# Kernel optimization log

Measured on AMD Instinct MI355X. Metric: run time of the kernel, lower is better.

Reference implementation:

```python
import jax, jax.numpy as jnp
import numpy as np

N_CRYST = 256   # number of crystals
A = 64          # atoms per crystal (uniform)
K = 20          # max_neighbors
HID = 128       # hidden_dim (emb_size_atom/edge)
LAT = 256       # latent_dim
NRBF = 128      # radial basis size
NBLK = 3        # interaction blocks
CUTOFF = 6.0    # radius
N_ATOMS = N_CRYST * A
E = N_ATOMS * K


def _lattice(lengths, angles):
    # lengths, angles: (N_cryst, 3); angles in degrees -> (N_cryst, 3, 3) row-vector lattice
    rad = angles * (np.pi / 180.0)
    cos = jnp.cos(rad)
    sg = jnp.sin(rad[:, 2])
    a, b, c = lengths[:, 0], lengths[:, 1], lengths[:, 2]
    cx = c * cos[:, 1]
    cy = c * (cos[:, 0] - cos[:, 1] * cos[:, 2]) / sg
    cz = jnp.sqrt(jnp.maximum(c ** 2 - cx ** 2 - cy ** 2, 1e-8))
    zeros = jnp.zeros_like(a)
    v1 = jnp.stack([a, zeros, zeros], -1)
    v2 = jnp.stack([b * cos[:, 2], b * sg, zeros], -1)
    v3 = jnp.stack([cx, cy, cz], -1)
    return jnp.stack([v1, v2, v3], axis=1)


def setup_inputs() -> dict:
    key = jax.random.key(0)
    ks = jax.random.split(key, 20)
    z = jax.random.normal(ks[0], (N_CRYST, LAT), jnp.float32)
    frac_coords = jax.random.uniform(ks[1], (N_ATOMS, 3), jnp.float32)
    lengths = 5.0 + 10.0 * jax.random.uniform(ks[2], (N_CRYST, 3), jnp.float32)
    angles = 60.0 + 60.0 * jax.random.uniform(ks[3], (N_CRYST, 3), jnp.float32)
    atom_types = jax.random.randint(ks[4], (N_ATOMS,), 1, 101)
    src = jnp.repeat(jnp.arange(N_ATOMS), K)
    dst = (src // A) * A + jax.random.randint(ks[5], (E,), 0, A)

    def w(k, shape, fan):
        return jax.random.normal(k, shape, jnp.float32) / np.sqrt(fan)

    params = dict(
        emb_table=w(ks[6], (101, HID), 1.0),
        W_in=w(ks[7], (HID + LAT, HID), HID + LAT), b_in=jnp.zeros((HID,), jnp.float32),
        W_edge=w(ks[8], (2 * HID + NRBF, HID), 2 * HID + NRBF), b_edge=jnp.zeros((HID,), jnp.float32),
        Wb_rbf=w(ks[9], (NBLK, NRBF, HID), NRBF),
        Wb_msg=w(ks[10], (NBLK, HID, HID), HID), bb_msg=jnp.zeros((NBLK, HID), jnp.float32),
        Wb_atom=w(ks[11], (NBLK, HID, HID), HID), bb_atom=jnp.zeros((NBLK, HID), jnp.float32),
        Wb_upd=w(ks[12], (NBLK, 3 * HID, HID), 3 * HID), bb_upd=jnp.zeros((NBLK, HID), jnp.float32),
        W_force=w(ks[13], (HID, 1), HID), b_force=jnp.zeros((1,), jnp.float32),
        W_fc1=w(ks[14], (HID, HID), HID), b_fc1=jnp.zeros((HID,), jnp.float32),
        W_fc2=w(ks[15], (HID, HID), HID), b_fc2=jnp.zeros((HID,), jnp.float32),
        W_fc3=w(ks[16], (HID, 2), HID), b_fc3=jnp.zeros((2,), jnp.float32),
    )
    return dict(z=z, frac_coords=frac_coords, lengths=lengths, angles=angles,
                atom_types=atom_types, src=src, dst=dst, **params)


def reference(z, frac_coords, lengths, angles,
              emb_table, W_in, b_in, W_edge, b_edge,
              Wb_rbf, Wb_msg, bb_msg, Wb_atom, bb_atom, Wb_upd, bb_upd,
              W_force, b_force, W_fc1, b_fc1, W_fc2, b_fc2, W_fc3, b_fc3,
              atom_types, src, dst):
    batch_idx = jnp.arange(N_ATOMS) // A  # crystal id per atom
    lattice = _lattice(lengths, angles)   # (N_cryst,3,3)
    cart = jnp.einsum('ni,nij->nj', frac_coords, lattice[batch_idx])  # (N_atoms,3)

    dvec = cart[dst] - cart[src]                        # (E,3)
    dist = jnp.sqrt(jnp.sum(dvec * dvec, -1) + 1e-12)    # (E,)
    unit = dvec / dist[:, None]

    mu = jnp.linspace(0.0, CUTOFF, NRBF)
    delta = CUTOFF / (NRBF - 1)
    env = 0.5 * (jnp.cos(np.pi * jnp.minimum(dist / CUTOFF, 1.0)) + 1.0)  # smooth cutoff
    rbf = jnp.exp(-(((dist[:, None] - mu) / delta) ** 2)) * env[:, None]   # (E,NRBF)

    # atom embedding conditioned on per-crystal latent
    h = jax.nn.relu(jnp.concatenate([emb_table[atom_types], z[batch_idx]], -1) @ W_in + b_in)
    # edge embedding
    m = jax.nn.relu(jnp.concatenate([h[src], h[dst], rbf], -1) @ W_edge + b_edge)

    for i in range(NBLK):
        gate = rbf @ Wb_rbf[i]                                   # (E,HID)
        msg = jax.nn.relu(m @ Wb_msg[i] + bb_msg[i]) * gate       # (E,HID)
        agg = jax.ops.segment_sum(msg, dst, num_segments=N_ATOMS) # (N_atoms,HID)
        h = h + jax.nn.relu(agg @ Wb_atom[i] + bb_atom[i])
        m = m + jax.nn.relu(jnp.concatenate([h[src], h[dst], m], -1) @ Wb_upd[i] + bb_upd[i])

    # per-edge force magnitude projected along edge direction, summed per atom
    f = m @ W_force + b_force                                     # (E,1)
    pred_cart_coord_diff = jax.ops.segment_sum(f * unit, dst, num_segments=N_ATOMS)  # (N_atoms,3)

    a1 = jax.nn.relu(h @ W_fc1 + b_fc1)
    a2 = jax.nn.relu(a1 @ W_fc2 + b_fc2)
    pred_atom_types = a2 @ W_fc3 + b_fc3                          # (N_atoms,2)
    return pred_cart_coord_diff, pred_atom_types
```

## Files before the change

### kernel.cpp

```cpp
#include <hip/hip_runtime.h>
#include <hip/hip_bf16.h>

#define NCRYST 256
#define AATOMS 64
#define KNBR   20
#define HID    128
#define LAT    256
#define NRBF   128
#define NBLK   3
#define NATOMS (NCRYST * AATOMS)
#define NEDGE  (NATOMS * KNBR)
#define NPART  2
#define DQ     4096
#define PI_F   3.14159265358979323846f
#define CUT_F  6.0f
#define CHB    1040

typedef short short8 __attribute__((ext_vector_type(8)));
typedef float f32x4  __attribute__((ext_vector_type(4)));

__device__ __forceinline__ float bf2f(__hip_bfloat16 x) { return __bfloat162float(x); }
__device__ __forceinline__ __hip_bfloat16 f2bf(float x) { return __float2bfloat16(x); }
__device__ __forceinline__ float s2f(short x) {
  return __uint_as_float(((unsigned)(unsigned short)x) << 16);
}
__device__ __forceinline__ short f2s(float x) {
  union { short s; __hip_bfloat16 b; } u; u.b = f2bf(x); return u.s;
}

#define DMA16(gptr, lptr) __builtin_amdgcn_global_load_lds( \
    (const __attribute__((address_space(1))) void*)(gptr),  \
    (__attribute__((address_space(3))) void*)(lptr), 16, 0, 0)

#define WCNT_VM11_LGKM0 0x007B
#define WCNT_VM10_LGKM0 0x007A
#define WCNT_VM4_LGKM0  0x0074
#define WCNT_VM0_LGKM0  0x0070
#define WCNT_LGKM0_ONLY 0xC07F

__global__ void k_cart(const float* __restrict__ frac, const float* __restrict__ lengths,
                       const float* __restrict__ angles, float* __restrict__ cart) {
  int atom = blockIdx.x * blockDim.x + threadIdx.x;
  if (atom >= NATOMS) return;
  int c = atom >> 6;
  float al = angles[c*3+0] * (PI_F/180.f);
  float be = angles[c*3+1] * (PI_F/180.f);
  float ga = angles[c*3+2] * (PI_F/180.f);
  float ca = cosf(al), cb = cosf(be), cg = cosf(ga), sg = sinf(ga);
  float a = lengths[c*3+0], b = lengths[c*3+1], cl = lengths[c*3+2];
  float cx = cl * cb;
  float cy = cl * (ca - cb*cg) / sg;
  float cz = sqrtf(fmaxf(cl*cl - cx*cx - cy*cy, 1e-8f));
  float f0 = frac[atom*3+0], f1 = frac[atom*3+1], f2 = frac[atom*3+2];
  cart[atom*3+0] = f0*a + f1*(b*cg) + f2*cx;
  cart[atom*3+1] = f1*(b*sg) + f2*cy;
  cart[atom*3+2] = f2*cz;
}

__global__ void k_edge(const float* __restrict__ cart, const int* __restrict__ src,
                       const int* __restrict__ dst, float* __restrict__ unit,
                       float* __restrict__ dist, const float* __restrict__ b_force,
                       float* __restrict__ fbuf) {
  int e = blockIdx.x * blockDim.x + threadIdx.x;
  if (e >= NEDGE) return;
  int s = src[e], d = dst[e];
  float dx = cart[d*3+0] - cart[s*3+0];
  float dy = cart[d*3+1] - cart[s*3+1];
  float dz = cart[d*3+2] - cart[s*3+2];
  float dd = sqrtf(dx*dx + dy*dy + dz*dz + 1e-12f);
  float inv = 1.f / dd;
  dist[e] = dd;
  unit[e*3+0] = dx*inv; unit[e*3+1] = dy*inv; unit[e*3+2] = dz*inv;
  fbuf[e] = b_force[0];
}

__global__ __launch_bounds__(128) void k_tab(const float* __restrict__ W_edge,
                                             const float* __restrict__ Wb_rbf,
                                             float* __restrict__ T) {
  int q = blockIdx.x, n = threadIdx.x;
  __shared__ float rv[128];
  float d = (float)q * (CUT_F / (float)(DQ - 1));
  float env = 0.5f * (cosf(PI_F * fminf(d * (1.f/CUT_F), 1.f)) + 1.f);
  float t = (d - (float)n * (CUT_F/(NRBF-1))) * ((NRBF-1)/CUT_F);
  rv[n] = expf(-t*t) * env;
  __syncthreads();
  float a0 = 0.f, a1 = 0.f, a2 = 0.f, a3 = 0.f;
  for (int j = 0; j < 128; ++j) {
    float r = rv[j];
    a0 = fmaf(r, W_edge[(256 + j)*128 + n], a0);
    a1 = fmaf(r, Wb_rbf[0*16384 + j*128 + n], a1);
    a2 = fmaf(r, Wb_rbf[1*16384 + j*128 + n], a2);
    a3 = fmaf(r, Wb_rbf[2*16384 + j*128 + n], a3);
  }
  T[(0*DQ + q)*128 + n] = a0;
  T[(1*DQ + q)*128 + n] = a1;
  T[(2*DQ + q)*128 + n] = a2;
  T[(3*DQ + q)*128 + n] = a3;
}

__global__ void k_wcast(const float* __restrict__ W_in, const float* __restrict__ W_edge,
                        const float* __restrict__ Wb_upd, const float* __restrict__ Wb_msg,
                        const float* __restrict__ Wb_atom, const float* __restrict__ W_fc1,
                        const float* __restrict__ W_fc2, __hip_bfloat16* __restrict__ WT) {
  int idx = blockIdx.x * 256 + threadIdx.x;
  if (idx >= 360448) return;
  if (idx < 49152) {
    int n = idx / 384, k = idx % 384;
    WT[idx] = f2bf(W_in[k*128 + n]);
    return;
  }
  int t = idx - 49152;
  int b = t >> 14, q = t & 16383;
  int n = q >> 7, k = q & 127;
  const float* S; int krow;
  if (b == 0)       { S = W_edge; krow = k; }
  else if (b == 1)  { S = W_edge; krow = 128 + k; }
  else if (b <= 10) { int i = (b-2)/3, part = (b-2)%3;
                      S = Wb_upd + i*49152; krow = part*128 + k; }
  else if (b <= 13) { S = Wb_msg + (b-11)*16384; krow = k; }
  else if (b <= 16) { S = Wb_atom + (b-14)*16384; krow = k; }
  else if (b == 17) { S = W_fc1; krow = k; }
  else              { S = W_fc2; krow = k; }
  WT[idx] = f2bf(S[krow*128 + n]);
}

__global__ __launch_bounds__(256) void k_hm(
    const int* __restrict__ atype, const float* __restrict__ z,
    const float* __restrict__ emb, const __hip_bfloat16* __restrict__ WTin,
    const float* __restrict__ b, float* __restrict__ h,
    __hip_bfloat16* __restrict__ h_bf) {
  const int tid = threadIdx.x;
  const int w = tid >> 6, lane = tid & 63, ln = lane & 15, qd = lane >> 4;
  const int row0w = blockIdx.x * 64 + w * 16;
  const int arow = row0w + ln;
  const float* esrc = emb + (size_t)atype[arow] * 128;
  const float* zsrc = z + (size_t)(arow >> 6) * LAT;

  short8 af[12];
#pragma unroll
  for (int ks = 0; ks < 4; ++ks) {
    float4 v0 = *(const float4*)(esrc + ks*32 + qd*8);
    float4 v1 = *(const float4*)(esrc + ks*32 + qd*8 + 4);
    af[ks] = (short8){f2s(v0.x),f2s(v0.y),f2s(v0.z),f2s(v0.w),
                      f2s(v1.x),f2s(v1.y),f2s(v1.z),f2s(v1.w)};
  }
#pragma unroll
  for (int ks = 4; ks < 12; ++ks) {
    float4 v0 = *(const float4*)(zsrc + (ks-4)*32 + qd*8);
    float4 v1 = *(const float4*)(zsrc + (ks-4)*32 + qd*8 + 4);
    af[ks] = (short8){f2s(v0.x),f2s(v0.y),f2s(v0.z),f2s(v0.w),
                      f2s(v1.x),f2s(v1.y),f2s(v1.z),f2s(v1.w)};
  }

  const short* Wb = (const short*)WTin + ln*384 + qd*8;
  f32x4 acc[8];
#pragma unroll
  for (int ct = 0; ct < 8; ++ct) acc[ct] = (f32x4){0,0,0,0};
#pragma unroll
  for (int ks = 0; ks < 12; ++ks)
#pragma unroll
    for (int ct = 0; ct < 8; ++ct)
      acc[ct] = __builtin_amdgcn_mfma_f32_16x16x32_bf16(af[ks],
                  *(const short8*)(Wb + ct*16*384 + ks*32), acc[ct], 0,0,0);

#pragma unroll
  for (int ct = 0; ct < 8; ++ct) {
    int col = ct*16 + ln;
    float bias = b[col];
#pragma unroll
    for (int reg = 0; reg < 4; ++reg) {
      int crow = row0w + qd*4 + reg;
      float v = fmaxf(acc[ct][reg] + bias, 0.f);
      size_t o = (size_t)crow*128 + col;
      h[o] = v;
      h_bf[o] = f2bf(v);
    }
  }
}

__global__ __launch_bounds__(256) void k_uv2(
    const __hip_bfloat16* __restrict__ A,
    const __hip_bfloat16* __restrict__ WT1, const __hip_bfloat16* __restrict__ WT2,
    __hip_bfloat16* __restrict__ O1, __hip_bfloat16* __restrict__ O2) {
  const int tid = threadIdx.x;
  const int w = tid >> 6, lane = tid & 63, ln = lane & 15, qd = lane >> 4;
  const int row0w = blockIdx.x * 64 + w * 16;
  const int arow = row0w + ln;

  short8 af[4];
  const short* pa = (const short*)A + (size_t)arow*128 + qd*8;
#pragma unroll
  for (int ks = 0; ks < 4; ++ks) af[ks] = *(const short8*)(pa + ks*32);

  f32x4 a1[8], a2[8];
#pragma unroll
  for (int ct = 0; ct < 8; ++ct) { a1[ct] = (f32x4){0,0,0,0}; a2[ct] = (f32x4){0,0,0,0}; }
#pragma unroll
  for (int ct = 0; ct < 8; ++ct) {
    const short* b1 = (const short*)WT1 + (ct*16 + ln)*128 + qd*8;
    const short* b2 = (const short*)WT2 + (ct*16 + ln)*128 + qd*8;
#pragma unroll
    for (int ks = 0; ks < 4; ++ks) {
      a1[ct] = __builtin_amdgcn_mfma_f32_16x16x32_bf16(af[ks], *(const short8*)(b1 + ks*32), a1[ct], 0,0,0);
      a2[ct] = __builtin_amdgcn_mfma_f32_16x16x32_bf16(af[ks], *(const short8*)(b2 + ks*32), a2[ct], 0,0,0);
    }
  }
#pragma unroll
  for (int ct = 0; ct < 8; ++ct) {
    int col = ct*16 + ln;
#pragma unroll
    for (int reg = 0; reg < 4; ++reg) {
      size_t o = (size_t)(row0w + qd*4 + reg)*128 + col;
      O1[o] = f2bf(a1[ct][reg]);
      O2[o] = f2bf(a2[ct][reg]);
    }
  }
}

__global__ __launch_bounds__(256) void k_minit(
    const int* __restrict__ src, const int* __restrict__ dst,
    const float* __restrict__ dist,
    const __hip_bfloat16* __restrict__ u0, const __hip_bfloat16* __restrict__ v0,
    const float* __restrict__ T0, const float* __restrict__ b,
    __hip_bfloat16* __restrict__ m) {
  const int t = threadIdx.x;
  const int li = t & 15, ei = t >> 4;
  float bcol[8];
#pragma unroll
  for (int u = 0; u < 8; ++u) bcol[u] = b[li*8 + u];

  int e[4]; float dd[4]; short8 us[4], vs[4];
#pragma unroll
  for (int g = 0; g < 4; ++g) {
    e[g] = blockIdx.x*64 + g*16 + ei;
    dd[g] = dist[e[g]];
    int s = src[e[g]], d = dst[e[g]];
    us[g] = *(const short8*)((const short*)u0 + (size_t)s*128 + li*8);
    vs[g] = *(const short8*)((const short*)v0 + (size_t)d*128 + li*8);
  }
  float t0v[4][8], t1v[4][8]; float fr[4]; bool in[4];
#pragma unroll
  for (int g = 0; g < 4; ++g) {
    in[g] = dd[g] < CUT_F;
    float x = fminf(dd[g], CUT_F) * ((float)(DQ - 1) / CUT_F);
    int i0 = (int)x;
    fr[g] = x - (float)i0;
    const float* tp = T0 + (size_t)i0*128 + li*8;
    *(float4*)&t0v[g][0] = *(const float4*)tp;
    *(float4*)&t0v[g][4] = *(const float4*)(tp + 4);
    *(float4*)&t1v[g][0] = *(const float4*)(tp + 128);
    *(float4*)&t1v[g][4] = *(const float4*)(tp + 132);
  }
#pragma unroll
  for (int g = 0; g < 4; ++g) {
    short8 o;
#pragma unroll
    for (int u = 0; u < 8; ++u) {
      float tv = in[g] ? fmaf(fr[g], t1v[g][u] - t0v[g][u], t0v[g][u]) : 0.f;
      float v = s2f(us[g][u]) + s2f(vs[g][u]) + tv + bcol[u];
      o[u] = f2s(fmaxf(v, 0.f));
    }
    *(uint4*)((short*)m + (size_t)e[g]*128 + li*8) = *(uint4*)&o;
  }
}

template<int MODE>
__global__ __launch_bounds__(256) void k_eup(
    const int* __restrict__ src, const int* __restrict__ dst,
    __hip_bfloat16* __restrict__ m,
    const __hip_bfloat16* __restrict__ uu, const __hip_bfloat16* __restrict__ vv,
    const __hip_bfloat16* __restrict__ WTmm, const float* __restrict__ b,
    const float* __restrict__ Wf, float* __restrict__ fout) {
  __shared__ short Bs[128 * 132];
  __shared__ __align__(16) char Abuf[2][17 * CHB];
  __shared__ short srcS[640], dstS[640];
  const int tid = threadIdx.x;
  const int w = tid >> 6, lane = tid & 63, ln = lane & 15, qd = lane >> 4;
  const int cg = w & 1, rh = w >> 1;
  const int e_loc = lane >> 4;
  const int sgc = (lane & 15) ^ (e_loc << 2);
  const int cry = blockIdx.x >> 1, half = blockIdx.x & 1;
  const int ebase = cry * 1280 + half * 640;
  const int ca = cry * 64;

#pragma unroll
  for (int i = 0; i < 8; ++i) {
    int g = i * 256 + tid;
    int colb = g >> 4, ch = g & 15;
    *(uint4*)&Bs[colb*132 + ch*8] = ((const uint4*)((const short*)WTmm + colb*128))[ch];
  }
  for (int i = tid; i < 640; i += 256) {
    srcS[i] = (short)(src[ebase + i] & 63);
    dstS[i] = (short)(dst[ebase + i] & 63);
  }

  float bias4[4], wf4[4];
#pragma unroll
  for (int ct = 0; ct < 4; ++ct) bias4[ct] = b[cg*64 + ct*16 + ln];
  if constexpr (MODE == 2) {
#pragma unroll
    for (int ct = 0; ct < 4; ++ct) wf4[ct] = Wf[cg*64 + ct*16 + ln];
  }

  short8 Bu[2][4], Bv[2][4];
#pragma unroll
  for (int ks = 0; ks < 2; ++ks)
#pragma unroll
    for (int ct = 0; ct < 4; ++ct) {
      const int col = cg*64 + ct*16 + ln;
#pragma unroll
      for (int j = 0; j < 8; ++j) {
        const size_t ro = (size_t)(ca + ks*32 + qd*8 + j) * 128 + col;
        Bu[ks][ct][j] = ((const short*)uu)[ro];
        Bv[ks][ct][j] = ((const short*)vv)[ro];
      }
    }

#pragma unroll
  for (int t4 = 0; t4 < 4; ++t4) {
    int chunk = w * 4 + t4;
    const short* gp = (const short*)m + (size_t)(ebase + chunk*4 + e_loc)*128 + sgc*8;
    DMA16(gp, Abuf[0] + chunk * CHB);
  }

  for (int t = 0; t < 10; ++t) {
    const int nb = t & 1;
    if (t < 9) {
#pragma unroll
      for (int t4 = 0; t4 < 4; ++t4) {
        int chunk = w * 4 + t4;
        const short* gp = (const short*)m +
            (size_t)(ebase + (t+1)*64 + chunk*4 + e_loc)*128 + sgc*8;
        DMA16(gp, Abuf[nb^1] + chunk * CHB);
      }
      __builtin_amdgcn_s_waitcnt(WCNT_VM4_LGKM0);
    } else {
      __builtin_amdgcn_s_waitcnt(WCNT_VM0_LGKM0);
    }
    __builtin_amdgcn_s_barrier();

    const char* Ab = Abuf[nb];
    const int e0 = ebase + t*64;
    const int l0 = t*64;

    const int rowA = rh*32 + ln, rowB = rowA + 16;
    const int sa = srcS[l0 + rowA], da = dstS[l0 + rowA];
    const int sb = srcS[l0 + rowB], db = dstS[l0 + rowB];

    f32x4 acc0[4], acc1[4];
#pragma unroll
    for (int ct = 0; ct < 4; ++ct) { acc0[ct] = (f32x4){0,0,0,0}; acc1[ct] = (f32x4){0,0,0,0}; }
    const int sx = (ln & 3) << 2;
#pragma unroll
    for (int ks = 0; ks < 4; ++ks) {
      int slot = ((ks*4 + qd) ^ sx) << 4;
      short8 aA = *(const short8*)(Ab + (rowA>>2)*CHB + (ln&3)*256 + slot);
      short8 aB = *(const short8*)(Ab + (rowB>>2)*CHB + (ln&3)*256 + slot);
#pragma unroll
      for (int ct = 0; ct < 4; ++ct) {
        short8 bb = *(const short8*)&Bs[(cg*64 + ct*16 + ln)*132 + ks*32 + qd*8];
        acc0[ct] = __builtin_amdgcn_mfma_f32_16x16x32_bf16(aA, bb, acc0[ct], 0,0,0);
        acc1[ct] = __builtin_amdgcn_mfma_f32_16x16x32_bf16(aB, bb, acc1[ct], 0,0,0);
      }
    }

#pragma unroll
    for (int ks = 0; ks < 2; ++ks) {
      short8 ohAu, ohAv, ohBu, ohBv;
#pragma unroll
      for (int j = 0; j < 8; ++j) {
        const int kk = ks*32 + qd*8 + j;
        ohAu[j] = (sa == kk) ? (short)0x3F80 : (short)0;
        ohAv[j] = (da == kk) ? (short)0x3F80 : (short)0;
        ohBu[j] = (sb == kk) ? (short)0x3F80 : (short)0;
        ohBv[j] = (db == kk) ? (short)0x3F80 : (short)0;
      }
#pragma unroll
      for (int ct = 0; ct < 4; ++ct) {
        acc0[ct] = __builtin_amdgcn_mfma_f32_16x16x32_bf16(ohAu, Bu[ks][ct], acc0[ct], 0,0,0);
        acc0[ct] = __builtin_amdgcn_mfma_f32_16x16x32_bf16(ohAv, Bv[ks][ct], acc0[ct], 0,0,0);
        acc1[ct] = __builtin_amdgcn_mfma_f32_16x16x32_bf16(ohBu, Bu[ks][ct], acc1[ct], 0,0,0);
        acc1[ct] = __builtin_amdgcn_mfma_f32_16x16x32_bf16(ohBv, Bv[ks][ct], acc1[ct], 0,0,0);
      }
    }

    float vreg[2][4][4];
#pragma unroll
    for (int mt = 0; mt < 2; ++mt) {
      const f32x4* acc = mt ? acc1 : acc0;
#pragma unroll
      for (int reg = 0; reg < 4; ++reg) {
        int lrow = rh*32 + mt*16 + qd*4 + reg;
        float fp = 0.f;
#pragma unroll
        for (int ct = 0; ct < 4; ++ct) {
          int col = cg*64 + ct*16 + ln;
          int colg = col >> 3;
          float res = s2f(*(const short*)(Ab + (lrow>>2)*CHB + (lrow&3)*256
                         + ((colg ^ ((lrow&3)<<2)) << 4) + (col&7)*2));
          float val = fmaxf(acc[ct][reg] + bias4[ct], 0.f) + res;
          if constexpr (MODE == 1) vreg[mt][reg][ct] = val;
          else fp = fmaf(val, wf4[ct], fp);
        }
        if constexpr (MODE == 2) {
          fp += __shfl_xor(fp, 1, 64);
          fp += __shfl_xor(fp, 2, 64);
          fp += __shfl_xor(fp, 4, 64);
          fp += __shfl_xor(fp, 8, 64);
          if (ln == 0) atomicAdd(&fout[e0 + lrow], fp);
        }
      }
    }

    if constexpr (MODE == 1) {
      __builtin_amdgcn_s_waitcnt(WCNT_LGKM0_ONLY);
      __builtin_amdgcn_s_barrier();
      short* res = (short*)Abuf[nb];
#pragma unroll
      for (int mt = 0; mt < 2; ++mt)
#pragma unroll
        for (int reg = 0; reg < 4; ++reg) {
          int lrow = rh*32 + mt*16 + qd*4 + reg;
#pragma unroll
          for (int ct = 0; ct < 4; ++ct)
            res[lrow*136 + cg*64 + ct*16 + ln] = f2s(vreg[mt][reg][ct]);
        }
      __builtin_amdgcn_s_waitcnt(WCNT_LGKM0_ONLY);
      __builtin_amdgcn_s_barrier();
#pragma unroll
      for (int i = 0; i < 4; ++i) {
        int g = i * 256 + tid;
        int row = g >> 4, ch = g & 15;
        *(uint4*)((short*)m + (size_t)(e0 + row)*128 + ch*8) =
            *(const uint4*)((const char*)Abuf[nb] + row*272 + ch*16);
      }
      __builtin_amdgcn_s_waitcnt(WCNT_LGKM0_ONLY);
      __builtin_amdgcn_s_barrier();
    } else {
      __builtin_amdgcn_s_waitcnt(WCNT_LGKM0_ONLY);
      __builtin_amdgcn_s_barrier();
    }
  }
}

__global__ __launch_bounds__(256, 3) void k_msgagg(
    const __hip_bfloat16* __restrict__ m, const float* __restrict__ dist,
    const __hip_bfloat16* __restrict__ WmT, const float* __restrict__ bm,
    const float* __restrict__ Tg, const int* __restrict__ dst,
    __hip_bfloat16* __restrict__ aggP) {
  __shared__ __align__(16) char gateraw[32 * 140 * 4];
  __shared__ __align__(16) char Mb[2][8 * CHB];
  __shared__ short Pt[128 * 40];
  __shared__ int dstS[640];
  float* gate = (float*)gateraw;
  const int tid = threadIdx.x;
  const int c  = blockIdx.x >> 1, pq = blockIdx.x & 1;
  const int w = tid >> 6, lane = tid & 63, ln = lane & 15, qd = lane >> 4;
  const int ei = tid >> 3, li = tid & 7;
  const int e_loc = lane >> 4;
  const int sgc = (lane & 15) ^ (e_loc << 2);
  const int sw8 = (ln & 3) << 3;

  const int ebase = c * 1280 + pq * 640;

  float bias2[2];
#pragma unroll
  for (int ct = 0; ct < 2; ++ct) bias2[ct] = bm[w*32 + ct*16 + ln];

  short8 Bf[2][4];
#pragma unroll
  for (int ct = 0; ct < 2; ++ct) {
    const short* bp = (const short*)WmT + (size_t)(w*32 + ct*16 + ln)*128 + qd*8;
#pragma unroll
    for (int ks = 0; ks < 4; ++ks) Bf[ct][ks] = *(const short8*)(bp + ks*32);
  }

  for (int i = tid; i < 640; i += 256) dstS[i] = dst[ebase + i] & 63;

  float4 ta[4], tb[4]; float frc, msk;
  {
    float d0 = dist[ebase + ei];
    msk = (d0 < CUT_F) ? 1.f : 0.f;
    float x = fminf(d0, CUT_F) * ((float)(DQ - 1) / CUT_F);
    int i0 = (int)x; if (i0 > DQ-2) i0 = DQ-2;
    frc = x - (float)i0;
    const float* tp = Tg + (size_t)i0*128 + li*16;
#pragma unroll
    for (int j = 0; j < 4; ++j) {
      ta[j] = *(const float4*)(tp + j*4);
      tb[j] = *(const float4*)(tp + 128 + j*4);
    }
  }
  float dn = dist[ebase + 32 + ei];
#pragma unroll
  for (int t = 0; t < 2; ++t) {
    int chunk = w*2 + t;
    const short* gp = (const short*)m + (size_t)(ebase + chunk*4 + e_loc)*128 + sgc*8;
    DMA16(gp, Mb[0] + chunk*CHB);
  }
#pragma unroll
  for (int j = 0; j < 4; ++j) {
    float4 g;
    g.x = msk * fmaf(frc, tb[j].x - ta[j].x, ta[j].x);
    g.y = msk * fmaf(frc, tb[j].y - ta[j].y, ta[j].y);
    g.z = msk * fmaf(frc, tb[j].z - ta[j].z, ta[j].z);
    g.w = msk * fmaf(frc, tb[j].w - ta[j].w, ta[j].w);
    *(float4*)&gate[ei*140 + li*16 + j*4] = g;
  }
  __builtin_amdgcn_s_waitcnt(WCNT_LGKM0_ONLY);
  __builtin_amdgcn_s_barrier();

  f32x4 accA[4][2];
#pragma unroll
  for (int rt = 0; rt < 4; ++rt)
#pragma unroll
    for (int ct = 0; ct < 2; ++ct) accA[rt][ct] = (f32x4){0,0,0,0};

  for (int s = 0; s < 20; ++s) {
    const int e0 = ebase + s*32;

    if (s < 19) {
      msk = (dn < CUT_F) ? 1.f : 0.f;
      float x = fminf(dn, CUT_F) * ((float)(DQ - 1) / CUT_F);
      int i0 = (int)x; if (i0 > DQ-2) i0 = DQ-2;
      frc = x - (float)i0;
      const float* tp = Tg + (size_t)i0*128 + li*16;
#pragma unroll
      for (int j = 0; j < 4; ++j) {
        ta[j] = *(const float4*)(tp + j*4);
        tb[j] = *(const float4*)(tp + 128 + j*4);
      }
#pragma unroll
      for (int t = 0; t < 2; ++t) {
        int chunk = w*2 + t;
        const short* gp = (const short*)m + (size_t)(e0 + 32 + chunk*4 + e_loc)*128 + sgc*8;
        DMA16(gp, Mb[(s+1) & 1] + chunk*CHB);
      }
      if (s < 18) {
        dn = dist[e0 + 64 + ei];
        __builtin_amdgcn_s_waitcnt(WCNT_VM11_LGKM0);
      } else {
        __builtin_amdgcn_s_waitcnt(WCNT_VM10_LGKM0);
      }
    } else {
      __builtin_amdgcn_s_waitcnt(WCNT_VM0_LGKM0);
    }
    __builtin_amdgcn_s_barrier();

    const char* Ms = Mb[s & 1];
    short8 am[2][4];
#pragma unroll
    for (int et = 0; et < 2; ++et) {
      int r = et*16 + ln;
      const char* rp = Ms + (r>>2)*CHB + (r&3)*256;
      const int sx = (r & 3) << 2;
#pragma unroll
      for (int ks = 0; ks < 4; ++ks)
        am[et][ks] = *(const short8*)(rp + (((ks*4 + qd) ^ sx) << 4));
    }

    f32x4 acc[2][2];
#pragma unroll
    for (int et = 0; et < 2; ++et)
#pragma unroll
      for (int ct = 0; ct < 2; ++ct) acc[et][ct] = (f32x4){0,0,0,0};
#pragma unroll
    for (int ks = 0; ks < 4; ++ks)
#pragma unroll
      for (int et = 0; et < 2; ++et)
#pragma unroll
        for (int ct = 0; ct < 2; ++ct)
          acc[et][ct] = __builtin_amdgcn_mfma_f32_16x16x32_bf16(
              am[et][ks], Bf[ct][ks], acc[et][ct], 0,0,0);

#pragma unroll
    for (int et = 0; et < 2; ++et)
#pragma unroll
      for (int ct = 0; ct < 2; ++ct) {
        const int col = w*32 + ct*16 + ln;
        float p[4];
#pragma unroll
        for (int reg = 0; reg < 4; ++reg) {
          const int erow = et*16 + qd*4 + reg;
          p[reg] = fmaxf(acc[et][ct][reg] + bias2[ct], 0.f) * gate[erow*140 + col];
        }
        unsigned u01 = (unsigned)(unsigned short)f2s(p[0]) |
                       ((unsigned)(unsigned short)f2s(p[1]) << 16);
        unsigned u23 = (unsigned)(unsigned short)f2s(p[2]) |
                       ((unsigned)(unsigned short)f2s(p[3]) << 16);
        const int a0 = col*40 + ((et*16 + qd*4) ^ sw8);
        *(unsigned*)&Pt[a0]     = u01;
        *(unsigned*)&Pt[a0 + 2] = u23;
      }
    __builtin_amdgcn_s_waitcnt(WCNT_LGKM0_ONLY);
    __builtin_amdgcn_s_barrier();

    int dvj[8];
#pragma unroll
    for (int j = 0; j < 8; ++j) dvj[j] = dstS[s*32 + qd*8 + j];
    short8 pb0 = *(const short8*)&Pt[(w*32 + 0*16 + ln)*40 + ((qd*8) ^ sw8)];
    short8 pb1 = *(const short8*)&Pt[(w*32 + 1*16 + ln)*40 + ((qd*8) ^ sw8)];
#pragma unroll
    for (int rt = 0; rt < 4; ++rt) {
      short8 oh;
#pragma unroll
      for (int j = 0; j < 8; ++j)
        oh[j] = (dvj[j] == rt*16 + ln) ? (short)0x3F80 : (short)0;
      accA[rt][0] = __builtin_amdgcn_mfma_f32_16x16x32_bf16(oh, pb0, accA[rt][0], 0,0,0);
      accA[rt][1] = __builtin_amdgcn_mfma_f32_16x16x32_bf16(oh, pb1, accA[rt][1], 0,0,0);
    }

    if (s < 19) {
#pragma unroll
      for (int j = 0; j < 4; ++j) {
        float4 g;
        g.x = msk * fmaf(frc, tb[j].x - ta[j].x, ta[j].x);
        g.y = msk * fmaf(frc, tb[j].y - ta[j].y, ta[j].y);
        g.z = msk * fmaf(frc, tb[j].z - ta[j].z, ta[j].z);
        g.w = msk * fmaf(frc, tb[j].w - ta[j].w, ta[j].w);
        *(float4*)&gate[ei*140 + li*16 + j*4] = g;
      }
    }
  }

  short* tbuf = (short*)gateraw;
#pragma unroll
  for (int rt = 0; rt < 4; ++rt)
#pragma unroll
    for (int ct = 0; ct < 2; ++ct) {
      const int col = w*32 + ct*16 + ln;
#pragma unroll
      for (int reg = 0; reg < 4; ++reg)
        tbuf[(rt*16 + qd*4 + reg)*140 + col] = f2s(accA[rt][ct][reg]);
    }
  __builtin_amdgcn_s_waitcnt(WCNT_LGKM0_ONLY);
  __builtin_amdgcn_s_barrier();
  {
    __hip_bfloat16* outp = aggP + ((size_t)pq * NATOMS + c * 64) * HID;
    const int r = tid >> 2, cq = tid & 3;
#pragma unroll
    for (int hh = 0; hh < 4; ++hh) {
      short8 o = *(const short8*)&tbuf[r*140 + cq*32 + hh*8];
      *(uint4*)((short*)outp + (size_t)r*HID + cq*32 + hh*8) = *(uint4*)&o;
    }
  }
}

__global__ __launch_bounds__(256) void k_fcuv(
    const __hip_bfloat16* __restrict__ slices,
    const __hip_bfloat16* __restrict__ WTa, const float* __restrict__ ba,
    float* __restrict__ h, __hip_bfloat16* __restrict__ h_bf,
    const __hip_bfloat16* __restrict__ WTu, const __hip_bfloat16* __restrict__ WTv,
    __hip_bfloat16* __restrict__ uo, __hip_bfloat16* __restrict__ vo) {
  __shared__ short ht[64 * 136];
  const int tid = threadIdx.x;
  const int w = tid >> 6, lane = tid & 63, ln = lane & 15, qd = lane >> 4;
  const int row0w = blockIdx.x * 64 + w * 16;
  const int arow = row0w + ln;

  short8 af[4];
#pragma unroll
  for (int ks = 0; ks < 4; ++ks) {
    float s[8] = {0,0,0,0,0,0,0,0};
#pragma unroll
    for (int p = 0; p < NPART; ++p) {
      short8 v = *(const short8*)((const short*)slices +
                   (size_t)p*NATOMS*128 + (size_t)arow*128 + qd*8 + ks*32);
#pragma unroll
      for (int u = 0; u < 8; ++u) s[u] += s2f(v[u]);
    }
    af[ks] = (short8){f2s(s[0]),f2s(s[1]),f2s(s[2]),f2s(s[3]),
                      f2s(s[4]),f2s(s[5]),f2s(s[6]),f2s(s[7])};
  }

  const short* Wb = (const short*)WTa + ln*128 + qd*8;
  f32x4 acc[8];
#pragma unroll
  for (int ct = 0; ct < 8; ++ct) acc[ct] = (f32x4){0,0,0,0};
#pragma unroll
  for (int ct = 0; ct < 8; ++ct)
#pragma unroll
    for (int ks = 0; ks < 4; ++ks)
      acc[ct] = __builtin_amdgcn_mfma_f32_16x16x32_bf16(af[ks],
                  *(const short8*)(Wb + ct*16*128 + ks*32), acc[ct], 0,0,0);

#pragma unroll
  for (int ct = 0; ct < 8; ++ct) {
    int col = ct*16 + ln;
    float bias = ba[col];
#pragma unroll
    for (int reg = 0; reg < 4; ++reg) {
      int lrow = w*16 + qd*4 + reg;
      size_t o = (size_t)(blockIdx.x*64 + lrow)*128 + col;
      float v = fmaxf(acc[ct][reg] + bias, 0.f) + h[o];
      h[o] = v;
      short hb = f2s(v);
      h_bf[o] = *(__hip_bfloat16*)&hb;
      ht[lrow*136 + col] = hb;
    }
  }
  __syncthreads();

  short8 ah[4];
  const short* ph = &ht[(w*16 + ln)*136 + qd*8];
#pragma unroll
  for (int ks = 0; ks < 4; ++ks) ah[ks] = *(const short8*)(ph + ks*32);

  f32x4 a1[8], a2[8];
#pragma unroll
  for (int ct = 0; ct < 8; ++ct) { a1[ct] = (f32x4){0,0,0,0}; a2[ct] = (f32x4){0,0,0,0}; }
#pragma unroll
  for (int ct = 0; ct < 8; ++ct) {
    const short* b1 = (const short*)WTu + (ct*16 + ln)*128 + qd*8;
    const short* b2 = (const short*)WTv + (ct*16 + ln)*128 + qd*8;
#pragma unroll
    for (int ks = 0; ks < 4; ++ks) {
      a1[ct] = __builtin_amdgcn_mfma_f32_16x16x32_bf16(ah[ks], *(const short8*)(b1 + ks*32), a1[ct], 0,0,0);
      a2[ct] = __builtin_amdgcn_mfma_f32_16x16x32_bf16(ah[ks], *(const short8*)(b2 + ks*32), a2[ct], 0,0,0);
    }
  }
#pragma unroll
  for (int ct = 0; ct < 8; ++ct) {
    int col = ct*16 + ln;
#pragma unroll
    for (int reg = 0; reg < 4; ++reg) {
      size_t o = (size_t)(row0w + qd*4 + reg)*128 + col;
      uo[o] = f2bf(a1[ct][reg]);
      vo[o] = f2bf(a2[ct][reg]);
    }
  }
}

__global__ __launch_bounds__(256) void k_head(
    const __hip_bfloat16* __restrict__ h_bf,
    const __hip_bfloat16* __restrict__ WT1, const float* __restrict__ b1,
    const __hip_bfloat16* __restrict__ WT2, const float* __restrict__ b2,
    const float* __restrict__ W3, const float* __restrict__ b3,
    float* __restrict__ out) {
  __shared__ short t1[64 * 136];
  const int tid = threadIdx.x;
  const int w = tid >> 6, lane = tid & 63, ln = lane & 15, qd = lane >> 4;
  const int row0w = blockIdx.x * 64 + w * 16;
  const int arow = row0w + ln;

  short8 af[4];
  const short* pa = (const short*)h_bf + (size_t)arow*128 + qd*8;
#pragma unroll
  for (int ks = 0; ks < 4; ++ks) af[ks] = *(const short8*)(pa + ks*32);

  f32x4 acc[8];
#pragma unroll
  for (int ct = 0; ct < 8; ++ct) acc[ct] = (f32x4){0,0,0,0};
#pragma unroll
  for (int ct = 0; ct < 8; ++ct) {
    const short* bb = (const short*)WT1 + (ct*16 + ln)*128 + qd*8;
#pragma unroll
    for (int ks = 0; ks < 4; ++ks)
      acc[ct] = __builtin_amdgcn_mfma_f32_16x16x32_bf16(af[ks],
                  *(const short8*)(bb + ks*32), acc[ct], 0,0,0);
  }
#pragma unroll
  for (int ct = 0; ct < 8; ++ct) {
    int col = ct*16 + ln;
    float bias = b1[col];
#pragma unroll
    for (int reg = 0; reg < 4; ++reg) {
      int lrow = w*16 + qd*4 + reg;
      t1[lrow*136 + col] = f2s(fmaxf(acc[ct][reg] + bias, 0.f));
    }
  }
  __syncthreads();

  short8 a1f[4];
  const short* p1 = &t1[(w*16 + ln)*136 + qd*8];
#pragma unroll
  for (int ks = 0; ks < 4; ++ks) a1f[ks] = *(const short8*)(p1 + ks*32);

  f32x4 acc2[8];
#pragma unroll
  for (int ct = 0; ct < 8; ++ct) acc2[ct] = (f32x4){0,0,0,0};
#pragma unroll
  for (int ct = 0; ct < 8; ++ct) {
    const short* bb = (const short*)WT2 + (ct*16 + ln)*128 + qd*8;
#pragma unroll
    for (int ks = 0; ks < 4; ++ks)
      acc2[ct] = __builtin_amdgcn_mfma_f32_16x16x32_bf16(a1f[ks],
                   *(const short8*)(bb + ks*32), acc2[ct], 0,0,0);
  }

  float w3a[8], w3b[8];
#pragma unroll
  for (int ct = 0; ct < 8; ++ct) {
    int col = ct*16 + ln;
    w3a[ct] = W3[col*2+0];
    w3b[ct] = W3[col*2+1];
  }
#pragma unroll
  for (int reg = 0; reg < 4; ++reg) {
    float p0 = 0.f, p1v = 0.f;
#pragma unroll
    for (int ct = 0; ct < 8; ++ct) {
      float a2v = fmaxf(acc2[ct][reg] + b2[ct*16 + ln], 0.f);
      p0  = fmaf(a2v, w3a[ct], p0);
      p1v = fmaf(a2v, w3b[ct], p1v);
    }
    p0  += __shfl_xor(p0, 1, 64);  p1v += __shfl_xor(p1v, 1, 64);
    p0  += __shfl_xor(p0, 2, 64);  p1v += __shfl_xor(p1v, 2, 64);
    p0  += __shfl_xor(p0, 4, 64);  p1v += __shfl_xor(p1v, 4, 64);
    p0  += __shfl_xor(p0, 8, 64);  p1v += __shfl_xor(p1v, 8, 64);
    if (ln == 0) {
      int row = row0w + qd*4 + reg;
      out[row*2+0] = p0 + b3[0];
      out[row*2+1] = p1v + b3[1];
    }
  }
}

__global__ void k_pcart(const float* __restrict__ f, const float* __restrict__ unit,
                        const int* __restrict__ dst, float* __restrict__ out) {
  __shared__ float acc[AATOMS * 3];
  int c = blockIdx.x, tid = threadIdx.x;
  if (tid < AATOMS*3) acc[tid] = 0.f;
  __syncthreads();
  for (int t = tid; t < 1280; t += 256) {
    int e = c*1280 + t;
    int d = dst[e] & 63;
    float fv = f[e];
    atomicAdd(&acc[d*3+0], fv * unit[e*3+0]);
    atomicAdd(&acc[d*3+1], fv * unit[e*3+1]);
    atomicAdd(&acc[d*3+2], fv * unit[e*3+2]);
  }
  __syncthreads();
  if (tid < AATOMS*3) out[c*AATOMS*3 + tid] = acc[tid];
}

extern "C" void kernel_launch(void* const* d_in, const int* in_sizes, int n_in,
                              void* d_out, int out_size, void* d_ws, size_t ws_size,
                              hipStream_t stream) {
  const float* z        = (const float*)d_in[0];
  const float* frac     = (const float*)d_in[1];
  const float* lengths  = (const float*)d_in[2];
  const float* angles   = (const float*)d_in[3];
  const int*   atype    = (const int*)  d_in[4];
  const int*   src      = (const int*)  d_in[5];
  const int*   dst      = (const int*)  d_in[6];
  const float* emb      = (const float*)d_in[7];
  const float* W_in     = (const float*)d_in[8];
  const float* b_in     = (const float*)d_in[9];
  const float* W_edge   = (const float*)d_in[10];
  const float* b_edge   = (const float*)d_in[11];
  const float* Wb_rbf   = (const float*)d_in[12];
  const float* Wb_msg   = (const float*)d_in[13];
  const float* bb_msg   = (const float*)d_in[14];
  const float* Wb_atom  = (const float*)d_in[15];
  const float* bb_atom  = (const float*)d_in[16];
  const float* Wb_upd   = (const float*)d_in[17];
  const float* bb_upd   = (const float*)d_in[18];
  const float* W_force  = (const float*)d_in[19];
  const float* b_force  = (const float*)d_in[20];
  const float* W_fc1    = (const float*)d_in[21];
  const float* b_fc1    = (const float*)d_in[22];
  const float* W_fc2    = (const float*)d_in[23];
  const float* b_fc2    = (const float*)d_in[24];
  const float* W_fc3    = (const float*)d_in[25];
  const float* b_fc3    = (const float*)d_in[26];

  char* p = (char*)d_ws;
  float* cart = (float*)p;            p += (size_t)NATOMS*3*4;
  float* unit = (float*)p;            p += (size_t)NEDGE*3*4;
  float* dist = (float*)p;            p += (size_t)NEDGE*4;
  float* h    = (float*)p;            p += (size_t)NATOMS*HID*4;
  float* fbuf = (float*)p;            p += (size_t)NEDGE*4;
  float* T    = (float*)p;            p += (size_t)4*DQ*128*4;
  __hip_bfloat16* h_bf = (__hip_bfloat16*)p; p += (size_t)NATOMS*HID*2;
  __hip_bfloat16* u0t  = (__hip_bfloat16*)p; p += (size_t)NATOMS*HID*2;
  __hip_bfloat16* v0t  = (__hip_bfloat16*)p; p += (size_t)NATOMS*HID*2;
  __hip_bfloat16* uut  = (__hip_bfloat16*)p; p += (size_t)NATOMS*HID*2;
  __hip_bfloat16* vvt  = (__hip_bfloat16*)p; p += (size_t)NATOMS*HID*2;
  __hip_bfloat16* aggP = (__hip_bfloat16*)p; p += (size_t)NPART*NATOMS*HID*2;
  __hip_bfloat16* m    = (__hip_bfloat16*)p; p += (size_t)NEDGE*HID*2;
  __hip_bfloat16* WT   = (__hip_bfloat16*)p; p += (size_t)360448*2;

  __hip_bfloat16* WT_in   = WT;
  __hip_bfloat16* WTK     = WT + 49152;
  __hip_bfloat16* WT_u0   = WTK + 0*16384;
  __hip_bfloat16* WT_v0   = WTK + 1*16384;
  __hip_bfloat16* WT_updB = WTK + 2*16384;
  __hip_bfloat16* WT_msg  = WTK + 11*16384;
  __hip_bfloat16* WT_atom = WTK + 14*16384;
  __hip_bfloat16* WT_fc1  = WTK + 17*16384;
  __hip_bfloat16* WT_fc2  = WTK + 18*16384;

  float* out_cart = (float*)d_out;
  float* out_at   = out_cart + NATOMS*3;

  k_wcast<<<1408, 256, 0, stream>>>(W_in, W_edge, Wb_upd, Wb_msg, Wb_atom,
                                    W_fc1, W_fc2, WT);
  k_tab<<<DQ, 128, 0, stream>>>(W_edge, Wb_rbf, T);
  k_cart<<<NATOMS/256, 256, 0, stream>>>(frac, lengths, angles, cart);
  k_edge<<<NEDGE/256, 256, 0, stream>>>(cart, src, dst, unit, dist, b_force, fbuf);
  k_hm<<<NATOMS/64, 256, 0, stream>>>(atype, z, emb, WT_in, b_in, h, h_bf);
  k_uv2<<<NATOMS/64, 256, 0, stream>>>(h_bf, WT_u0, WT_v0, u0t, v0t);
  k_minit<<<NEDGE/64, 256, 0, stream>>>(src, dst, dist, u0t, v0t, T, b_edge, m);

  for (int i = 0; i < NBLK; ++i) {
    k_msgagg<<<NCRYST*NPART, 256, 0, stream>>>(m, dist, WT_msg + i*16384,
                                               bb_msg + i*HID, T + (size_t)(1+i)*DQ*128,
                                               dst, aggP);
    k_fcuv<<<NATOMS/64, 256, 0, stream>>>(aggP, WT_atom + i*16384, bb_atom + i*HID,
                                          h, h_bf,
                                          WT_updB + (3*i+0)*16384,
                                          WT_updB + (3*i+1)*16384, uut, vvt);
    if (i < NBLK-1) {
      k_eup<1><<<NCRYST*2, 256, 0, stream>>>(src, dst, m, uut, vvt,
                                             WT_updB + (3*i+2)*16384, bb_upd + i*HID,
                                             nullptr, nullptr);
    } else {
      k_eup<2><<<NCRYST*2, 256, 0, stream>>>(src, dst, m, uut, vvt,
                                             WT_updB + (3*i+2)*16384, bb_upd + i*HID,
                                             W_force, fbuf);
    }
  }
  k_pcart<<<NCRYST, 256, 0, stream>>>(fbuf, unit, dst, out_cart);
  k_head<<<NATOMS/64, 256, 0, stream>>>(h_bf, WT_fc1, b_fc1, WT_fc2, b_fc2,
                                        W_fc3, b_fc3, out_at);
}
```

Measured before the change: 604.2 us.

## Make gate buffer wave-private and drop mid-iteration barrier in msgagg

The shared gate buffer becomes per-wave: each wave computes only the gate columns its own MFMA tile consumes, so the gate no longer needs cross-wave sharing. This lets the block-wide barrier after the Pt write become a scheduling barrier, on the basis that each wave reads back only its own Pt columns. The DMA prefetch of the next m tile is issued after the top-of-loop barrier, which protects the double buffer from being overwritten while still being read, and waitcnt thresholds are adjusted to match. This cuts one workgroup barrier per step, at the cost of less lead time for the m prefetch and a smaller, wave-private LDS layout.

```diff
diff --git a/kernel.cpp b/kernel.cpp
--- a/kernel.cpp
+++ b/kernel.cpp
@@ -32,8 +32,8 @@
     (const __attribute__((address_space(1))) void*)(gptr),  \
     (__attribute__((address_space(3))) void*)(lptr), 16, 0, 0)
 
-#define WCNT_VM11_LGKM0 0x007B
-#define WCNT_VM10_LGKM0 0x007A
+#define WCNT_VM9_LGKM0  0x0079
+#define WCNT_VM8_LGKM0  0x0078
 #define WCNT_VM4_LGKM0  0x0074
 #define WCNT_VM0_LGKM0  0x0070
 #define WCNT_LGKM0_ONLY 0xC07F
@@ -448,19 +448,20 @@
     const __hip_bfloat16* __restrict__ WmT, const float* __restrict__ bm,
     const float* __restrict__ Tg, const int* __restrict__ dst,
     __hip_bfloat16* __restrict__ aggP) {
-  __shared__ __align__(16) char gateraw[32 * 140 * 4];
+  __shared__ __align__(16) char gateraw[4 * 32 * 36 * 4];
   __shared__ __align__(16) char Mb[2][8 * CHB];
   __shared__ short Pt[128 * 40];
   __shared__ int dstS[640];
-  float* gate = (float*)gateraw;
   const int tid = threadIdx.x;
   const int c  = blockIdx.x >> 1, pq = blockIdx.x & 1;
   const int w = tid >> 6, lane = tid & 63, ln = lane & 15, qd = lane >> 4;
-  const int ei = tid >> 3, li = tid & 7;
+  const int er = lane & 31, ch = lane >> 5;
   const int e_loc = lane >> 4;
   const int sgc = (lane & 15) ^ (e_loc << 2);
   const int sw8 = (ln & 3) << 3;
 
+  float* gateW = (float*)gateraw + w * 32 * 36;
+
   const int ebase = c * 1280 + pq * 640;
 
   float bias2[2];
@@ -479,24 +480,17 @@
 
   float4 ta[4], tb[4]; float frc, msk;
   {
-    float d0 = dist[ebase + ei];
+    float d0 = dist[ebase + er];
     msk = (d0 < CUT_F) ? 1.f : 0.f;
     float x = fminf(d0, CUT_F) * ((float)(DQ - 1) / CUT_F);
     int i0 = (int)x; if (i0 > DQ-2) i0 = DQ-2;
     frc = x - (float)i0;
-    const float* tp = Tg + (size_t)i0*128 + li*16;
+    const float* tp = Tg + (size_t)i0*128 + w*32 + ch*16;
 #pragma unroll
     for (int j = 0; j < 4; ++j) {
       ta[j] = *(const float4*)(tp + j*4);
       tb[j] = *(const float4*)(tp + 128 + j*4);
     }
-  }
-  float dn = dist[ebase + 32 + ei];
-#pragma unroll
-  for (int t = 0; t < 2; ++t) {
-    int chunk = w*2 + t;
-    const short* gp = (const short*)m + (size_t)(ebase + chunk*4 + e_loc)*128 + sgc*8;
-    DMA16(gp, Mb[0] + chunk*CHB);
   }
 #pragma unroll
   for (int j = 0; j < 4; ++j) {
@@ -505,7 +499,14 @@
     g.y = msk * fmaf(frc, tb[j].y - ta[j].y, ta[j].y);
     g.z = msk * fmaf(frc, tb[j].z - ta[j].z, ta[j].z);
     g.w = msk * fmaf(frc, tb[j].w - ta[j].w, ta[j].w);
-    *(float4*)&gate[ei*140 + li*16 + j*4] = g;
+    *(float4*)&gateW[er*36 + ch*16 + j*4] = g;
+  }
+  float dn = dist[ebase + 32 + er];
+#pragma unroll
+  for (int t = 0; t < 2; ++t) {
+    int chunk = w*2 + t;
+    const short* gp = (const short*)m + (size_t)(ebase + chunk*4 + e_loc)*128 + sgc*8;
+    DMA16(gp, Mb[0] + chunk*CHB);
   }
   __builtin_amdgcn_s_waitcnt(WCNT_LGKM0_ONLY);
   __builtin_amdgcn_s_barrier();
@@ -524,28 +525,31 @@
       float x = fminf(dn, CUT_F) * ((float)(DQ - 1) / CUT_F);
       int i0 = (int)x; if (i0 > DQ-2) i0 = DQ-2;
       frc = x - (float)i0;
-      const float* tp = Tg + (size_t)i0*128 + li*16;
+      const float* tp = Tg + (size_t)i0*128 + w*32 + ch*16;
 #pragma unroll
       for (int j = 0; j < 4; ++j) {
         ta[j] = *(const float4*)(tp + j*4);
         tb[j] = *(const float4*)(tp + 128 + j*4);
       }
+      if (s < 18) {
+        dn = dist[e0 + 64 + er];
+        __builtin_amdgcn_s_waitcnt(WCNT_VM9_LGKM0);
+      } else {
+        __builtin_amdgcn_s_waitcnt(WCNT_VM8_LGKM0);
+      }
+    } else {
+      __builtin_amdgcn_s_waitcnt(WCNT_VM0_LGKM0);
+    }
+    __builtin_amdgcn_s_barrier();
+
+    if (s < 19) {
 #pragma unroll
       for (int t = 0; t < 2; ++t) {
         int chunk = w*2 + t;
         const short* gp = (const short*)m + (size_t)(e0 + 32 + chunk*4 + e_loc)*128 + sgc*8;
         DMA16(gp, Mb[(s+1) & 1] + chunk*CHB);
       }
-      if (s < 18) {
-        dn = dist[e0 + 64 + ei];
-        __builtin_amdgcn_s_waitcnt(WCNT_VM11_LGKM0);
-      } else {
-        __builtin_amdgcn_s_waitcnt(WCNT_VM10_LGKM0);
-      }
-    } else {
-      __builtin_amdgcn_s_waitcnt(WCNT_VM0_LGKM0);
-    }
-    __builtin_amdgcn_s_barrier();
+    }
 
     const char* Ms = Mb[s & 1];
     short8 am[2][4];
@@ -582,7 +586,8 @@
 #pragma unroll
         for (int reg = 0; reg < 4; ++reg) {
           const int erow = et*16 + qd*4 + reg;
-          p[reg] = fmaxf(acc[et][ct][reg] + bias2[ct], 0.f) * gate[erow*140 + col];
+          p[reg] = fmaxf(acc[et][ct][reg] + bias2[ct], 0.f)
+                   * gateW[erow*36 + ct*16 + ln];
         }
         unsigned u01 = (unsigned)(unsigned short)f2s(p[0]) |
                        ((unsigned)(unsigned short)f2s(p[1]) << 16);
@@ -593,7 +598,7 @@
         *(unsigned*)&Pt[a0 + 2] = u23;
       }
     __builtin_amdgcn_s_waitcnt(WCNT_LGKM0_ONLY);
-    __builtin_amdgcn_s_barrier();
+    __builtin_amdgcn_sched_barrier(0);
 
     int dvj[8];
 #pragma unroll
@@ -618,11 +623,13 @@
         g.y = msk * fmaf(frc, tb[j].y - ta[j].y, ta[j].y);
         g.z = msk * fmaf(frc, tb[j].z - ta[j].z, ta[j].z);
         g.w = msk * fmaf(frc, tb[j].w - ta[j].w, ta[j].w);
-        *(float4*)&gate[ei*140 + li*16 + j*4] = g;
-      }
-    }
-  }
-
+        *(float4*)&gateW[er*36 + ch*16 + j*4] = g;
+      }
+    }
+  }
+
+  __builtin_amdgcn_s_waitcnt(WCNT_LGKM0_ONLY);
+  __builtin_amdgcn_s_barrier();
   short* tbuf = (short*)gateraw;
 #pragma unroll
   for (int rt = 0; rt < 4; ++rt)
```

After: 763.8 us. +26.4%, slower.
